# Kernel tuning notes

Measured on AMD Instinct MI355X. Metric: run time of the kernel, lower is better.

Reference implementation:

```python
import jax, jax.numpy as jnp
import numpy as np

NUM_GRAPHS = 4096
EPS = 1e-6

def _ln(x, g, b):
    mu = jnp.mean(x, axis=-1, keepdims=True)
    var = jnp.mean(jnp.square(x - mu), axis=-1, keepdims=True)
    return (x - mu) * jax.lax.rsqrt(var + EPS) * g + b

def setup_inputs() -> dict:
    key = jax.random.key(0)
    ks = jax.random.split(key, 8)
    N, D, H, DRUG = 262144, 128, 8, 128
    feat = jax.random.normal(ks[0], (N, D), dtype=jnp.float32)
    batch = jnp.sort(jax.random.randint(ks[1], (N,), 0, NUM_GRAPHS)).astype(jnp.int64)
    def lin(k, fi, fo):
        lim = 1.0 / np.sqrt(fi)
        return jax.random.uniform(k, (fi, fo), jnp.float32, -lim, lim)
    return {
        'feat': feat, 'batch': batch,
        'W1': lin(ks[2], D, 64), 'b1': jnp.zeros((64,), jnp.float32),
        'g1': jnp.ones((64,), jnp.float32), 'beta1': jnp.zeros((64,), jnp.float32),
        'W2': lin(ks[3], 64, H), 'b2': jnp.zeros((H,), jnp.float32),
        'W3': lin(ks[4], H * D, D), 'b3': jnp.zeros((D,), jnp.float32),
        'g3': jnp.ones((D,), jnp.float32), 'beta3': jnp.zeros((D,), jnp.float32),
        'W4': lin(ks[5], D, DRUG), 'b4': jnp.zeros((DRUG,), jnp.float32),
        'g4': jnp.ones((DRUG,), jnp.float32), 'beta4': jnp.zeros((DRUG,), jnp.float32),
    }

def reference(feat, batch, W1, b1, g1, beta1, W2, b2, W3, b3, g3, beta3, W4, b4, g4, beta4):
    seg = batch.astype(jnp.int32)
    # ATFC: Linear -> LeakyReLU -> LayerNorm -> Linear
    h = jax.nn.leaky_relu(feat @ W1 + b1)
    h = _ln(h, g1, beta1)
    att = jnp.exp(h @ W2 + b2)                      # [N, H]
    # segment softmax normalization
    s = jax.ops.segment_sum(att, seg, num_segments=NUM_GRAPHS)  # [B, H]
    att = att / s[seg]
    # weighted aggregation: outer product + segment sum -> [B, H, D]
    out = jax.ops.segment_sum(att[:, :, None] * feat[:, None, :], seg, num_segments=NUM_GRAPHS)
    out = out.reshape(NUM_GRAPHS, -1)               # [B, H*D]
    # output block (dropout is identity in eval mode)
    o = _ln(jax.nn.leaky_relu(out @ W3 + b3), g3, beta3)
    o = _ln(jax.nn.leaky_relu(o @ W4 + b4), g4, beta4)
    return o
```

## Files before the change

### kernel.cpp

```cpp
#include <hip/hip_runtime.h>
#include <math.h>

#define NG 4096
#define NN 262144
#define D 128
#define M1 64
#define NH 8
#define EPS 1e-6f

typedef __attribute__((ext_vector_type(8))) short short8;
typedef __attribute__((ext_vector_type(8))) unsigned char uchar8;
typedef __attribute__((ext_vector_type(4))) float f32x4;

__device__ inline float leaky(float x) { return x > 0.f ? x : 0.01f * x; }

__device__ inline short f2bf(float f) {
  union { float f; unsigned u; } v; v.f = f;
  unsigned r = (v.u + 0x7fffu + ((v.u >> 16) & 1u)) >> 16;
  return (short)r;
}
__device__ inline float bf2f(short s) {
  union { unsigned u; float f; } v;
  v.u = ((unsigned)(unsigned short)s) << 16;
  return v.f;
}

__global__ __launch_bounds__(256) void k0b_prep(
    const float* __restrict__ W3, const float* __restrict__ W4,
    short* __restrict__ W3T, short* __restrict__ W4T) {
  __shared__ float tile[64][65];
  int b = blockIdx.x, t = threadIdx.x;
  const float* src; short* dst; int kt, nt, tkl;
  if (b < 32) { src = W3; dst = W3T; kt = b >> 1; nt = b & 1; tkl = 1024; }
  else        { src = W4; dst = W4T; kt = (b - 32) >> 1; nt = (b - 32) & 1; tkl = 128; }

#pragma unroll
  for (int i = 0; i < 4; ++i) {
    int id = t + 256 * i;
    int r = id >> 4, c4 = (id & 15) * 4;
    float4 v = *(const float4*)(src + (size_t)(kt * 64 + r) * D + nt * 64 + c4);
    tile[r][c4 + 0] = v.x; tile[r][c4 + 1] = v.y;
    tile[r][c4 + 2] = v.z; tile[r][c4 + 3] = v.w;
  }
  __syncthreads();
  int n = t >> 2, kb = (t & 3) * 16;
  short8 p0, p1;
#pragma unroll
  for (int j = 0; j < 8; ++j) {
    p0[j] = f2bf(tile[kb + j][n]);
    p1[j] = f2bf(tile[kb + 8 + j][n]);
  }
  short* o = dst + (size_t)(nt * 64 + n) * tkl + kt * 64 + kb;
  *(short8*)o = p0;
  *(short8*)(o + 8) = p1;
}

__global__ __launch_bounds__(256) void k1_fused(
    const float* __restrict__ feat, const int* __restrict__ batch,
    const float* __restrict__ W1, const float* __restrict__ b1,
    const float* __restrict__ g1, const float* __restrict__ beta1,
    const float* __restrict__ W2, const float* __restrict__ b2,
    float* __restrict__ out_acc, float* __restrict__ s_sum) {
  __shared__ short W1T[M1][D + 8];
  __shared__ short W2T[16][M1 + 8];
  __shared__ short hb[128][72];
  __shared__ int batchL[128];
  __shared__ unsigned char giL[128];
  short (*attB)[136] = (short(*)[136])&hb[0][0];

  int t = threadIdx.x;
  int nb = blockIdx.x * 128;

#pragma unroll
  for (int i = 0; i < 8; ++i) {
    int idx4 = t + 256 * i;
    int k = idx4 >> 4;
    int j = (idx4 & 15) * 4;
    float4 wv = *(const float4*)(W1 + k * M1 + j);
    W1T[j + 0][k] = f2bf(wv.x);
    W1T[j + 1][k] = f2bf(wv.y);
    W1T[j + 2][k] = f2bf(wv.z);
    W1T[j + 3][k] = f2bf(wv.w);
  }
#pragma unroll
  for (int i = 0; i < 4; ++i) {
    int e = t * 4 + i;
    int hh = e >> 6, j = e & 63;
    W2T[hh][j] = (hh < NH) ? f2bf(W2[j * NH + hh]) : (short)0;
  }
  if (t < 128) batchL[t] = batch[nb + t];
  __syncthreads();

  int w = t >> 6, l = t & 63;
  int lr = l & 15, lq = l >> 4;
  int nbw = nb + w * 32;
  int g_lo = batchL[0], g_hi = batchL[127];

  short8 afr[2][4];
#pragma unroll
  for (int mt = 0; mt < 2; ++mt) {
    const float* rp = feat + (size_t)(nbw + mt * 16 + lr) * D + lq * 8;
#pragma unroll
    for (int c = 0; c < 4; ++c) {
      float4 x0 = *(const float4*)(rp + c * 32);
      float4 x1 = *(const float4*)(rp + c * 32 + 4);
      short8 a;
      a[0] = f2bf(x0.x); a[1] = f2bf(x0.y); a[2] = f2bf(x0.z); a[3] = f2bf(x0.w);
      a[4] = f2bf(x1.x); a[5] = f2bf(x1.y); a[6] = f2bf(x1.z); a[7] = f2bf(x1.w);
      afr[mt][c] = a;
    }
  }

  f32x4 acc[2][4];
#pragma unroll
  for (int mt = 0; mt < 2; ++mt)
#pragma unroll
    for (int nt = 0; nt < 4; ++nt) acc[mt][nt] = (f32x4){0.f, 0.f, 0.f, 0.f};
#pragma unroll
  for (int c = 0; c < 4; ++c) {
#pragma unroll
    for (int nt = 0; nt < 4; ++nt) {
      short8 bfr = *(const short8*)&W1T[nt * 16 + lr][c * 32 + lq * 8];
      acc[0][nt] = __builtin_amdgcn_mfma_f32_16x16x32_bf16(afr[0][c], bfr, acc[0][nt], 0, 0, 0);
      acc[1][nt] = __builtin_amdgcn_mfma_f32_16x16x32_bf16(afr[1][c], bfr, acc[1][nt], 0, 0, 0);
    }
  }

  float b1v[4], g1v[4], btv[4];
#pragma unroll
  for (int nt = 0; nt < 4; ++nt) {
    b1v[nt] = b1[nt * 16 + lr];
    g1v[nt] = g1[nt * 16 + lr];
    btv[nt] = beta1[nt * 16 + lr];
  }
#pragma unroll
  for (int mt = 0; mt < 2; ++mt) {
#pragma unroll
    for (int r = 0; r < 4; ++r) {
      float x[4], s1 = 0.f, s2 = 0.f;
#pragma unroll
      for (int nt = 0; nt < 4; ++nt) {
        float xv = leaky(acc[mt][nt][r] + b1v[nt]);
        x[nt] = xv;
        s1 += xv;
        s2 = fmaf(xv, xv, s2);
      }
#pragma unroll
      for (int off = 1; off < 16; off <<= 1) {
        s1 += __shfl_xor(s1, off);
        s2 += __shfl_xor(s2, off);
      }
      float mu = s1 * (1.f / M1);
      float var = s2 * (1.f / M1) - mu * mu;
      float inv = rsqrtf(var + EPS);
      int node = w * 32 + mt * 16 + lq * 4 + r;
#pragma unroll
      for (int nt = 0; nt < 4; ++nt)
        hb[node][nt * 16 + lr] = f2bf((x[nt] - mu) * inv * g1v[nt] + btv[nt]);
    }
  }
  __syncthreads();

  f32x4 acc2[2];
  acc2[0] = (f32x4){0.f, 0.f, 0.f, 0.f};
  acc2[1] = (f32x4){0.f, 0.f, 0.f, 0.f};
#pragma unroll
  for (int c2 = 0; c2 < 2; ++c2) {
    short8 bfr2 = *(const short8*)&W2T[lr][c2 * 32 + lq * 8];
#pragma unroll
    for (int mt = 0; mt < 2; ++mt) {
      short8 af2 = *(const short8*)&hb[w * 32 + mt * 16 + lr][c2 * 32 + lq * 8];
      acc2[mt] = __builtin_amdgcn_mfma_f32_16x16x32_bf16(af2, bfr2, acc2[mt], 0, 0, 0);
    }
  }
  __syncthreads();

  if (lr < NH) {
    float b2v = b2[lr];
    float attv[2][4];
    int bnode[2][4];
#pragma unroll
    for (int mt = 0; mt < 2; ++mt)
#pragma unroll
      for (int r = 0; r < 4; ++r) {
        int node = w * 32 + mt * 16 + lq * 4 + r;
        float av = bf2f(f2bf(expf(acc2[mt][r] + b2v)));
        attv[mt][r] = av;
        bnode[mt][r] = batchL[node];
        attB[lr][node] = f2bf(av);
      }
    for (int g = g_lo; g <= g_hi; ++g) {
      float ss = 0.f;
#pragma unroll
      for (int mt = 0; mt < 2; ++mt)
#pragma unroll
        for (int r = 0; r < 4; ++r)
          ss += (bnode[mt][r] == g) ? attv[mt][r] : 0.f;
      ss += __shfl_xor(ss, 16);
      ss += __shfl_xor(ss, 32);
      if (lq == 0) atomicAdd(s_sum + g * NH + lr, ss);
    }
  }
  if (t < 128) giL[t] = (unsigned char)(batchL[t] - g_lo);
  __syncthreads();

  short8 bfA[4], bfB[4];
#pragma unroll
  for (int kc = 0; kc < 4; ++kc) {
    int dA = w * 32 + lr, dB = w * 32 + 16 + lr;
    short8 ba, bb;
#pragma unroll
    for (int j = 0; j < 8; ++j) {
      const float* fp = feat + (size_t)(nb + kc * 32 + lq * 8 + j) * D;
      ba[j] = f2bf(fp[dA]);
      bb[j] = f2bf(fp[dB]);
    }
    bfA[kc] = ba;
    bfB[kc] = bb;
  }

  int hA = lr & 7;
  for (int gp = g_lo; gp <= g_hi; gp += 4) {
    int t0 = (gp - g_lo) + (lr >> 3);
    int t1 = t0 + 2;
    f32x4 aggc00 = (f32x4){0.f, 0.f, 0.f, 0.f};
    f32x4 aggc01 = (f32x4){0.f, 0.f, 0.f, 0.f};
    f32x4 aggc10 = (f32x4){0.f, 0.f, 0.f, 0.f};
    f32x4 aggc11 = (f32x4){0.f, 0.f, 0.f, 0.f};
#pragma unroll
    for (int kc = 0; kc < 4; ++kc) {
      short8 av = *(const short8*)&attB[hA][kc * 32 + lq * 8];
      uchar8 gv = *(const uchar8*)&giL[kc * 32 + lq * 8];
      short8 a0, a1;
#pragma unroll
      for (int j = 0; j < 8; ++j) {
        short x = av[j];
        a0[j] = (gv[j] == t0) ? x : (short)0;
        a1[j] = (gv[j] == t1) ? x : (short)0;
      }
      aggc00 = __builtin_amdgcn_mfma_f32_16x16x32_bf16(a0, bfA[kc], aggc00, 0, 0, 0);
      aggc01 = __builtin_amdgcn_mfma_f32_16x16x32_bf16(a0, bfB[kc], aggc01, 0, 0, 0);
      aggc10 = __builtin_amdgcn_mfma_f32_16x16x32_bf16(a1, bfA[kc], aggc10, 0, 0, 0);
      aggc11 = __builtin_amdgcn_mfma_f32_16x16x32_bf16(a1, bfB[kc], aggc11, 0, 0, 0);
    }

    int giC0 = gp + (lq >> 1);
    int giC1 = gp + 2 + (lq >> 1);
    int dA = w * 32 + lr, dB = w * 32 + 16 + lr;
    if (giC0 <= g_hi) {
      float* p0 = out_acc + (size_t)giC0 * (NH * D) + ((lq & 1) * 4) * D;
#pragma unroll
      for (int r = 0; r < 4; ++r) {
        atomicAdd(p0 + r * D + dA, aggc00[r]);
        atomicAdd(p0 + r * D + dB, aggc01[r]);
      }
    }
    if (giC1 <= g_hi) {
      float* p1 = out_acc + (size_t)giC1 * (NH * D) + ((lq & 1) * 4) * D;
#pragma unroll
      for (int r = 0; r < 4; ++r) {
        atomicAdd(p1 + r * D + dA, aggc10[r]);
        atomicAdd(p1 + r * D + dB, aggc11[r]);
      }
    }
  }
}

__global__ __launch_bounds__(128) void k3_mlp(
    const float* __restrict__ X, const float* __restrict__ s_sum,
    const short* __restrict__ W3T,
    const float* __restrict__ b3, const float* __restrict__ g3,
    const float* __restrict__ beta3, const short* __restrict__ W4T,
    const float* __restrict__ b4, const float* __restrict__ g4,
    const float* __restrict__ beta4, float* __restrict__ out) {
  __shared__ short hbuf[16][136];
  __shared__ float red[2][2][16];

  int t = threadIdx.x;
  int nw = t >> 6, l = t & 63;
  int lr = l & 15, lq = l >> 4;
  int gb = blockIdx.x * 16;

  float invs[8];
#pragma unroll
  for (int h = 0; h < 8; ++h) {
    float sv = s_sum[(gb + lr) * NH + h];
    invs[h] = sv > 0.f ? 1.f / sv : 0.f;
  }

  const float* xrow = X + (size_t)(gb + lr) * (NH * D) + lq * 8;
  f32x4 acc[4];
#pragma unroll
  for (int nt = 0; nt < 4; ++nt) acc[nt] = (f32x4){0.f, 0.f, 0.f, 0.f};

#pragma unroll
  for (int kc = 0; kc < 32; ++kc) {
    float4 x0 = *(const float4*)(xrow + kc * 32);
    float4 x1 = *(const float4*)(xrow + kc * 32 + 4);
    float inv = invs[kc >> 2];
    short8 a;
    a[0] = f2bf(x0.x * inv); a[1] = f2bf(x0.y * inv);
    a[2] = f2bf(x0.z * inv); a[3] = f2bf(x0.w * inv);
    a[4] = f2bf(x1.x * inv); a[5] = f2bf(x1.y * inv);
    a[6] = f2bf(x1.z * inv); a[7] = f2bf(x1.w * inv);
#pragma unroll
    for (int nt = 0; nt < 4; ++nt) {
      int ncol = nw * 64 + nt * 16 + lr;
      short8 b = *(const short8*)(W3T + (size_t)ncol * 1024 + kc * 32 + lq * 8);
      acc[nt] = __builtin_amdgcn_mfma_f32_16x16x32_bf16(a, b, acc[nt], 0, 0, 0);
    }
  }

  float xv[4][4], s1[4] = {0.f, 0.f, 0.f, 0.f}, s2[4] = {0.f, 0.f, 0.f, 0.f};
#pragma unroll
  for (int nt = 0; nt < 4; ++nt) {
    float bb = b3[nw * 64 + nt * 16 + lr];
#pragma unroll
    for (int r = 0; r < 4; ++r) {
      float v = leaky(acc[nt][r] + bb);
      xv[nt][r] = v;
      s1[r] += v;
      s2[r] = fmaf(v, v, s2[r]);
    }
  }
#pragma unroll
  for (int off = 1; off < 16; off <<= 1) {
#pragma unroll
    for (int r = 0; r < 4; ++r) {
      s1[r] += __shfl_xor(s1[r], off);
      s2[r] += __shfl_xor(s2[r], off);
    }
  }
  if (lr == 0) {
#pragma unroll
    for (int r = 0; r < 4; ++r) {
      red[nw][0][lq * 4 + r] = s1[r];
      red[nw][1][lq * 4 + r] = s2[r];
    }
  }
  __syncthreads();
#pragma unroll
  for (int nt = 0; nt < 4; ++nt) {
    int col = nw * 64 + nt * 16 + lr;
    float gg = g3[col], bt = beta3[col];
#pragma unroll
    for (int r = 0; r < 4; ++r) {
      int row = lq * 4 + r;
      float S1 = red[0][0][row] + red[1][0][row];
      float S2 = red[0][1][row] + red[1][1][row];
      float mu = S1 * (1.f / D);
      float var = S2 * (1.f / D) - mu * mu;
      float inv = rsqrtf(var + EPS);
      hbuf[row][col] = f2bf((xv[nt][r] - mu) * inv * gg + bt);
    }
  }
  __syncthreads();

  f32x4 acc2[4];
#pragma unroll
  for (int nt = 0; nt < 4; ++nt) acc2[nt] = (f32x4){0.f, 0.f, 0.f, 0.f};
#pragma unroll
  for (int kc = 0; kc < 4; ++kc) {
    short8 a2 = *(const short8*)&hbuf[lr][kc * 32 + lq * 8];
#pragma unroll
    for (int nt = 0; nt < 4; ++nt) {
      int ncol = nw * 64 + nt * 16 + lr;
      short8 b2 = *(const short8*)(W4T + (size_t)ncol * 128 + kc * 32 + lq * 8);
      acc2[nt] = __builtin_amdgcn_mfma_f32_16x16x32_bf16(a2, b2, acc2[nt], 0, 0, 0);
    }
  }

#pragma unroll
  for (int r = 0; r < 4; ++r) { s1[r] = 0.f; s2[r] = 0.f; }
#pragma unroll
  for (int nt = 0; nt < 4; ++nt) {
    float bb = b4[nw * 64 + nt * 16 + lr];
#pragma unroll
    for (int r = 0; r < 4; ++r) {
      float v = leaky(acc2[nt][r] + bb);
      xv[nt][r] = v;
      s1[r] += v;
      s2[r] = fmaf(v, v, s2[r]);
    }
  }
#pragma unroll
  for (int off = 1; off < 16; off <<= 1) {
#pragma unroll
    for (int r = 0; r < 4; ++r) {
      s1[r] += __shfl_xor(s1[r], off);
      s2[r] += __shfl_xor(s2[r], off);
    }
  }
  __syncthreads();
  if (lr == 0) {
#pragma unroll
    for (int r = 0; r < 4; ++r) {
      red[nw][0][lq * 4 + r] = s1[r];
      red[nw][1][lq * 4 + r] = s2[r];
    }
  }
  __syncthreads();
#pragma unroll
  for (int nt = 0; nt < 4; ++nt) {
    int col = nw * 64 + nt * 16 + lr;
    float gg = g4[col], bt = beta4[col];
#pragma unroll
    for (int r = 0; r < 4; ++r) {
      int row = lq * 4 + r;
      float S1 = red[0][0][row] + red[1][0][row];
      float S2 = red[0][1][row] + red[1][1][row];
      float mu = S1 * (1.f / D);
      float var = S2 * (1.f / D) - mu * mu;
      float inv = rsqrtf(var + EPS);
      out[(size_t)(gb + row) * D + col] = (xv[nt][r] - mu) * inv * gg + bt;
    }
  }
}

extern "C" void kernel_launch(void* const* d_in, const int* in_sizes, int n_in,
                              void* d_out, int out_size, void* d_ws, size_t ws_size,
                              hipStream_t stream) {
  (void)in_sizes; (void)n_in; (void)out_size; (void)ws_size;
  const float* feat  = (const float*)d_in[0];
  const int*   batch = (const int*)d_in[1];
  const float* W1    = (const float*)d_in[2];
  const float* b1    = (const float*)d_in[3];
  const float* g1    = (const float*)d_in[4];
  const float* beta1 = (const float*)d_in[5];
  const float* W2    = (const float*)d_in[6];
  const float* b2    = (const float*)d_in[7];
  const float* W3    = (const float*)d_in[8];
  const float* b3    = (const float*)d_in[9];
  const float* g3    = (const float*)d_in[10];
  const float* beta3 = (const float*)d_in[11];
  const float* W4    = (const float*)d_in[12];
  const float* b4    = (const float*)d_in[13];
  const float* g4    = (const float*)d_in[14];
  const float* beta4 = (const float*)d_in[15];
  float* out = (float*)d_out;

  char* ws = (char*)d_ws;
  float* out_acc = (float*)ws;
  float* s_sum   = (float*)(ws + (size_t)NG * NH * D * 4);
  char*  p       = ws + (size_t)NG * NH * D * 4 + (size_t)NG * NH * 4;
  short* W3T     = (short*)p;
  short* W4T     = (short*)(p + 262144);

  hipMemsetAsync(out_acc, 0, (size_t)NG * NH * D * 4 + (size_t)NG * NH * 4,
                 stream);
  k0b_prep<<<36, 256, 0, stream>>>(W3, W4, W3T, W4T);
  k1_fused<<<NN / 128, 256, 0, stream>>>(feat, batch, W1, b1, g1, beta1, W2, b2,
                                         out_acc, s_sum);
  k3_mlp<<<NG / 16, 128, 0, stream>>>(out_acc, s_sum, W3T, b3, g3, beta3, W4T,
                                      b4, g4, beta4, out);
}
```

Baseline: 261.4 us.

## Fuse segment aggregation and output MLP into one graph-partitioned kernel

Each block now owns 8 graphs, with segment start offsets found by binary search in the prep kernel. It walks that range's nodes in 128-node chunks and accumulates the softmax sums and the weighted aggregation in shared memory instead of global atomics. The W3/W4 MLP with its LayerNorms then runs in the same block, which removes the memset, the global out_acc round trip and a separate kernel launch. The cost is a large shared-memory footprint (about 34KB for agg alone), only 512 blocks, and chunk boundaries that do not line up with 128-node tiles, which leads to some redundant loads and padded work.

Result: slower. 268.0 us (+2.5%).

```diff
diff --git a/kernel.cpp b/kernel.cpp
--- a/kernel.cpp
+++ b/kernel.cpp
@@ -6,6 +6,7 @@
 #define D 128
 #define M1 64
 #define NH 8
+#define GPB 8
 #define EPS 1e-6f
 
 typedef __attribute__((ext_vector_type(8))) short short8;
@@ -27,9 +28,22 @@
 
 __global__ __launch_bounds__(256) void k0b_prep(
     const float* __restrict__ W3, const float* __restrict__ W4,
-    short* __restrict__ W3T, short* __restrict__ W4T) {
+    const int* __restrict__ batch,
+    short* __restrict__ W3T, short* __restrict__ W4T,
+    int* __restrict__ starts) {
   __shared__ float tile[64][65];
   int b = blockIdx.x, t = threadIdx.x;
+  if (b >= 36) {
+    int g = (b - 36) * 256 + t;
+    int lo = 0, hi = NN;
+    while (lo < hi) {
+      int mid = (lo + hi) >> 1;
+      if (batch[mid] < g) lo = mid + 1; else hi = mid;
+    }
+    starts[g] = lo;
+    if (g == 0) starts[NG] = NN;
+    return;
+  }
   const float* src; short* dst; int kt, nt, tkl;
   if (b < 32) { src = W3; dst = W3T; kt = b >> 1; nt = b & 1; tkl = 1024; }
   else        { src = W4; dst = W4T; kt = (b - 32) >> 1; nt = (b - 32) & 1; tkl = 128; }
@@ -55,27 +69,38 @@
   *(short8*)(o + 8) = p1;
 }
 
-__global__ __launch_bounds__(256) void k1_fused(
+__global__ __launch_bounds__(256, 2) void k_fused(
     const float* __restrict__ feat, const int* __restrict__ batch,
+    const int* __restrict__ starts,
     const float* __restrict__ W1, const float* __restrict__ b1,
     const float* __restrict__ g1, const float* __restrict__ beta1,
     const float* __restrict__ W2, const float* __restrict__ b2,
-    float* __restrict__ out_acc, float* __restrict__ s_sum) {
+    const short* __restrict__ W3T, const float* __restrict__ b3,
+    const float* __restrict__ g3, const float* __restrict__ beta3,
+    const short* __restrict__ W4T, const float* __restrict__ b4,
+    const float* __restrict__ g4, const float* __restrict__ beta4,
+    float* __restrict__ out) {
   __shared__ short W1T[M1][D + 8];
   __shared__ short W2T[16][M1 + 8];
   __shared__ short hb[128][72];
-  __shared__ int batchL[128];
-  __shared__ unsigned char giL[128];
+  __shared__ float agg[GPB][NH][D + 4];
+  __shared__ float sL[GPB][NH];
+  __shared__ unsigned char giL2[2][128];
+  __shared__ float red[4][2][16];
+  __shared__ short hbuf2[16][136];
+
   short (*attB)[136] = (short(*)[136])&hb[0][0];
+  short (*aL)[1040] = (short(*)[1040])&hb[0][0];
 
   int t = threadIdx.x;
-  int nb = blockIdx.x * 128;
+  int G0 = blockIdx.x * GPB;
+  int w = t >> 6, l = t & 63;
+  int lr = l & 15, lq = l >> 4;
 
 #pragma unroll
   for (int i = 0; i < 8; ++i) {
     int idx4 = t + 256 * i;
-    int k = idx4 >> 4;
-    int j = (idx4 & 15) * 4;
+    int k = idx4 >> 4, j = (idx4 & 15) * 4;
     float4 wv = *(const float4*)(W1 + k * M1 + j);
     W1T[j + 0][k] = f2bf(wv.x);
     W1T[j + 1][k] = f2bf(wv.y);
@@ -88,43 +113,8 @@
     int hh = e >> 6, j = e & 63;
     W2T[hh][j] = (hh < NH) ? f2bf(W2[j * NH + hh]) : (short)0;
   }
-  if (t < 128) batchL[t] = batch[nb + t];
-  __syncthreads();
-
-  int w = t >> 6, l = t & 63;
-  int lr = l & 15, lq = l >> 4;
-  int nbw = nb + w * 32;
-  int g_lo = batchL[0], g_hi = batchL[127];
-
-  short8 afr[2][4];
-#pragma unroll
-  for (int mt = 0; mt < 2; ++mt) {
-    const float* rp = feat + (size_t)(nbw + mt * 16 + lr) * D + lq * 8;
-#pragma unroll
-    for (int c = 0; c < 4; ++c) {
-      float4 x0 = *(const float4*)(rp + c * 32);
-      float4 x1 = *(const float4*)(rp + c * 32 + 4);
-      short8 a;
-      a[0] = f2bf(x0.x); a[1] = f2bf(x0.y); a[2] = f2bf(x0.z); a[3] = f2bf(x0.w);
-      a[4] = f2bf(x1.x); a[5] = f2bf(x1.y); a[6] = f2bf(x1.z); a[7] = f2bf(x1.w);
-      afr[mt][c] = a;
-    }
-  }
-
-  f32x4 acc[2][4];
-#pragma unroll
-  for (int mt = 0; mt < 2; ++mt)
-#pragma unroll
-    for (int nt = 0; nt < 4; ++nt) acc[mt][nt] = (f32x4){0.f, 0.f, 0.f, 0.f};
-#pragma unroll
-  for (int c = 0; c < 4; ++c) {
-#pragma unroll
-    for (int nt = 0; nt < 4; ++nt) {
-      short8 bfr = *(const short8*)&W1T[nt * 16 + lr][c * 32 + lq * 8];
-      acc[0][nt] = __builtin_amdgcn_mfma_f32_16x16x32_bf16(afr[0][c], bfr, acc[0][nt], 0, 0, 0);
-      acc[1][nt] = __builtin_amdgcn_mfma_f32_16x16x32_bf16(afr[1][c], bfr, acc[1][nt], 0, 0, 0);
-    }
-  }
+  for (int i = t; i < GPB * NH * (D + 4); i += 256) (&agg[0][0][0])[i] = 0.f;
+  if (t < GPB * NH) (&sL[0][0])[t] = 0.f;
 
   float b1v[4], g1v[4], btv[4];
 #pragma unroll
@@ -133,286 +123,311 @@
     g1v[nt] = g1[nt * 16 + lr];
     btv[nt] = beta1[nt * 16 + lr];
   }
-#pragma unroll
-  for (int mt = 0; mt < 2; ++mt) {
-#pragma unroll
-    for (int r = 0; r < 4; ++r) {
-      float x[4], s1 = 0.f, s2 = 0.f;
+  float b2v = b2[lr & 7];
+
+  int s0 = starts[G0], s1 = starts[G0 + GPB];
+  int nchunks = (s1 - s0 + 127) >> 7;
+
+  for (int c = 0; c < nchunks; ++c) {
+    int base = s0 + (c << 7);
+    int nvalid = min(128, s1 - base);
+    unsigned char* gi = giL2[c & 1];
+    if (t < 128)
+      gi[t] = (t < nvalid) ? (unsigned char)(batch[base + t] - G0)
+                           : (unsigned char)255;
+
+    short8 afr[2][4];
+#pragma unroll
+    for (int mt = 0; mt < 2; ++mt) {
+      int node = base + w * 32 + mt * 16 + lr;
+      node = node < NN ? node : NN - 1;
+      const float* rp = feat + (size_t)node * D + lq * 8;
+#pragma unroll
+      for (int cc = 0; cc < 4; ++cc) {
+        float4 x0 = *(const float4*)(rp + cc * 32);
+        float4 x1 = *(const float4*)(rp + cc * 32 + 4);
+        short8 a;
+        a[0] = f2bf(x0.x); a[1] = f2bf(x0.y); a[2] = f2bf(x0.z); a[3] = f2bf(x0.w);
+        a[4] = f2bf(x1.x); a[5] = f2bf(x1.y); a[6] = f2bf(x1.z); a[7] = f2bf(x1.w);
+        afr[mt][cc] = a;
+      }
+    }
+    __syncthreads();
+
+    f32x4 acc[2][4];
+#pragma unroll
+    for (int mt = 0; mt < 2; ++mt)
+#pragma unroll
+      for (int nt = 0; nt < 4; ++nt) acc[mt][nt] = (f32x4){0.f, 0.f, 0.f, 0.f};
+#pragma unroll
+    for (int cc = 0; cc < 4; ++cc) {
 #pragma unroll
       for (int nt = 0; nt < 4; ++nt) {
-        float xv = leaky(acc[mt][nt][r] + b1v[nt]);
-        x[nt] = xv;
-        s1 += xv;
-        s2 = fmaf(xv, xv, s2);
-      }
-#pragma unroll
-      for (int off = 1; off < 16; off <<= 1) {
-        s1 += __shfl_xor(s1, off);
-        s2 += __shfl_xor(s2, off);
-      }
-      float mu = s1 * (1.f / M1);
-      float var = s2 * (1.f / M1) - mu * mu;
-      float inv = rsqrtf(var + EPS);
-      int node = w * 32 + mt * 16 + lq * 4 + r;
-#pragma unroll
-      for (int nt = 0; nt < 4; ++nt)
-        hb[node][nt * 16 + lr] = f2bf((x[nt] - mu) * inv * g1v[nt] + btv[nt]);
-    }
-  }
-  __syncthreads();
-
-  f32x4 acc2[2];
-  acc2[0] = (f32x4){0.f, 0.f, 0.f, 0.f};
-  acc2[1] = (f32x4){0.f, 0.f, 0.f, 0.f};
-#pragma unroll
-  for (int c2 = 0; c2 < 2; ++c2) {
-    short8 bfr2 = *(const short8*)&W2T[lr][c2 * 32 + lq * 8];
+        short8 bfr = *(const short8*)&W1T[nt * 16 + lr][cc * 32 + lq * 8];
+        acc[0][nt] = __builtin_amdgcn_mfma_f32_16x16x32_bf16(afr[0][cc], bfr, acc[0][nt], 0, 0, 0);
+        acc[1][nt] = __builtin_amdgcn_mfma_f32_16x16x32_bf16(afr[1][cc], bfr, acc[1][nt], 0, 0, 0);
+      }
+    }
+
 #pragma unroll
     for (int mt = 0; mt < 2; ++mt) {
-      short8 af2 = *(const short8*)&hb[w * 32 + mt * 16 + lr][c2 * 32 + lq * 8];
-      acc2[mt] = __builtin_amdgcn_mfma_f32_16x16x32_bf16(af2, bfr2, acc2[mt], 0, 0, 0);
-    }
-  }
-  __syncthreads();
-
-  if (lr < NH) {
-    float b2v = b2[lr];
-    float attv[2][4];
-    int bnode[2][4];
-#pragma unroll
-    for (int mt = 0; mt < 2; ++mt)
 #pragma unroll
       for (int r = 0; r < 4; ++r) {
+        float x[4], sa = 0.f, sb = 0.f;
+#pragma unroll
+        for (int nt = 0; nt < 4; ++nt) {
+          float xvv = leaky(acc[mt][nt][r] + b1v[nt]);
+          x[nt] = xvv; sa += xvv; sb = fmaf(xvv, xvv, sb);
+        }
+#pragma unroll
+        for (int off = 1; off < 16; off <<= 1) {
+          sa += __shfl_xor(sa, off);
+          sb += __shfl_xor(sb, off);
+        }
+        float mu = sa * (1.f / M1);
+        float var = sb * (1.f / M1) - mu * mu;
+        float inv = rsqrtf(var + EPS);
         int node = w * 32 + mt * 16 + lq * 4 + r;
-        float av = bf2f(f2bf(expf(acc2[mt][r] + b2v)));
-        attv[mt][r] = av;
-        bnode[mt][r] = batchL[node];
-        attB[lr][node] = f2bf(av);
-      }
-    for (int g = g_lo; g <= g_hi; ++g) {
-      float ss = 0.f;
+#pragma unroll
+        for (int nt = 0; nt < 4; ++nt)
+          hb[node][nt * 16 + lr] = f2bf((x[nt] - mu) * inv * g1v[nt] + btv[nt]);
+      }
+    }
+    __syncthreads();
+
+    f32x4 acc2[2];
+    acc2[0] = (f32x4){0.f, 0.f, 0.f, 0.f};
+    acc2[1] = (f32x4){0.f, 0.f, 0.f, 0.f};
+#pragma unroll
+    for (int c2 = 0; c2 < 2; ++c2) {
+      short8 bfr2 = *(const short8*)&W2T[lr][c2 * 32 + lq * 8];
+#pragma unroll
+      for (int mt = 0; mt < 2; ++mt) {
+        short8 af2 = *(const short8*)&hb[w * 32 + mt * 16 + lr][c2 * 32 + lq * 8];
+        acc2[mt] = __builtin_amdgcn_mfma_f32_16x16x32_bf16(af2, bfr2, acc2[mt], 0, 0, 0);
+      }
+    }
+    __syncthreads();
+
+    int gl_lo = gi[0];
+    int gl_hi = gi[nvalid - 1];
+
+    if (lr < NH) {
+      float attv[2][4];
+      int gnode[2][4];
 #pragma unroll
       for (int mt = 0; mt < 2; ++mt)
 #pragma unroll
-        for (int r = 0; r < 4; ++r)
-          ss += (bnode[mt][r] == g) ? attv[mt][r] : 0.f;
-      ss += __shfl_xor(ss, 16);
-      ss += __shfl_xor(ss, 32);
-      if (lq == 0) atomicAdd(s_sum + g * NH + lr, ss);
-    }
-  }
-  if (t < 128) giL[t] = (unsigned char)(batchL[t] - g_lo);
-  __syncthreads();
-
-  short8 bfA[4], bfB[4];
-#pragma unroll
-  for (int kc = 0; kc < 4; ++kc) {
-    int dA = w * 32 + lr, dB = w * 32 + 16 + lr;
-    short8 ba, bb;
-#pragma unroll
-    for (int j = 0; j < 8; ++j) {
-      const float* fp = feat + (size_t)(nb + kc * 32 + lq * 8 + j) * D;
-      ba[j] = f2bf(fp[dA]);
-      bb[j] = f2bf(fp[dB]);
-    }
-    bfA[kc] = ba;
-    bfB[kc] = bb;
-  }
-
-  int hA = lr & 7;
-  for (int gp = g_lo; gp <= g_hi; gp += 4) {
-    int t0 = (gp - g_lo) + (lr >> 3);
-    int t1 = t0 + 2;
-    f32x4 aggc00 = (f32x4){0.f, 0.f, 0.f, 0.f};
-    f32x4 aggc01 = (f32x4){0.f, 0.f, 0.f, 0.f};
-    f32x4 aggc10 = (f32x4){0.f, 0.f, 0.f, 0.f};
-    f32x4 aggc11 = (f32x4){0.f, 0.f, 0.f, 0.f};
+        for (int r = 0; r < 4; ++r) {
+          int node = w * 32 + mt * 16 + lq * 4 + r;
+          float av = bf2f(f2bf(expf(acc2[mt][r] + b2v)));
+          attv[mt][r] = av;
+          gnode[mt][r] = gi[node];
+          attB[lr][node] = f2bf(av);
+        }
+      for (int g = gl_lo; g <= gl_hi; ++g) {
+        float ss = 0.f;
+#pragma unroll
+        for (int mt = 0; mt < 2; ++mt)
+#pragma unroll
+          for (int r = 0; r < 4; ++r)
+            ss += (gnode[mt][r] == g) ? attv[mt][r] : 0.f;
+        ss += __shfl_xor(ss, 16);
+        ss += __shfl_xor(ss, 32);
+        if (lq == 0) atomicAdd(&sL[g][lr], ss);
+      }
+    }
+    __syncthreads();
+
+    int dA = w * 32 + lr, dB = dA + 16;
+    short8 bfA[4], bfB[4];
 #pragma unroll
     for (int kc = 0; kc < 4; ++kc) {
-      short8 av = *(const short8*)&attB[hA][kc * 32 + lq * 8];
-      uchar8 gv = *(const uchar8*)&giL[kc * 32 + lq * 8];
-      short8 a0, a1;
+      short8 ba, bb;
 #pragma unroll
       for (int j = 0; j < 8; ++j) {
-        short x = av[j];
-        a0[j] = (gv[j] == t0) ? x : (short)0;
-        a1[j] = (gv[j] == t1) ? x : (short)0;
-      }
-      aggc00 = __builtin_amdgcn_mfma_f32_16x16x32_bf16(a0, bfA[kc], aggc00, 0, 0, 0);
-      aggc01 = __builtin_amdgcn_mfma_f32_16x16x32_bf16(a0, bfB[kc], aggc01, 0, 0, 0);
-      aggc10 = __builtin_amdgcn_mfma_f32_16x16x32_bf16(a1, bfA[kc], aggc10, 0, 0, 0);
-      aggc11 = __builtin_amdgcn_mfma_f32_16x16x32_bf16(a1, bfB[kc], aggc11, 0, 0, 0);
-    }
-
-    int giC0 = gp + (lq >> 1);
-    int giC1 = gp + 2 + (lq >> 1);
-    int dA = w * 32 + lr, dB = w * 32 + 16 + lr;
-    if (giC0 <= g_hi) {
-      float* p0 = out_acc + (size_t)giC0 * (NH * D) + ((lq & 1) * 4) * D;
-#pragma unroll
-      for (int r = 0; r < 4; ++r) {
-        atomicAdd(p0 + r * D + dA, aggc00[r]);
-        atomicAdd(p0 + r * D + dB, aggc01[r]);
-      }
-    }
-    if (giC1 <= g_hi) {
-      float* p1 = out_acc + (size_t)giC1 * (NH * D) + ((lq & 1) * 4) * D;
-#pragma unroll
-      for (int r = 0; r < 4; ++r) {
-        atomicAdd(p1 + r * D + dA, aggc10[r]);
-        atomicAdd(p1 + r * D + dB, aggc11[r]);
-      }
-    }
-  }
-}
-
-__global__ __launch_bounds__(128) void k3_mlp(
-    const float* __restrict__ X, const float* __restrict__ s_sum,
-    const short* __restrict__ W3T,
-    const float* __restrict__ b3, const float* __restrict__ g3,
-    const float* __restrict__ beta3, const short* __restrict__ W4T,
-    const float* __restrict__ b4, const float* __restrict__ g4,
-    const float* __restrict__ beta4, float* __restrict__ out) {
-  __shared__ short hbuf[16][136];
-  __shared__ float red[2][2][16];
-
-  int t = threadIdx.x;
-  int nw = t >> 6, l = t & 63;
-  int lr = l & 15, lq = l >> 4;
-  int gb = blockIdx.x * 16;
-
-  float invs[8];
-#pragma unroll
-  for (int h = 0; h < 8; ++h) {
-    float sv = s_sum[(gb + lr) * NH + h];
-    invs[h] = sv > 0.f ? 1.f / sv : 0.f;
-  }
-
-  const float* xrow = X + (size_t)(gb + lr) * (NH * D) + lq * 8;
-  f32x4 acc[4];
-#pragma unroll
-  for (int nt = 0; nt < 4; ++nt) acc[nt] = (f32x4){0.f, 0.f, 0.f, 0.f};
-
+        int node = base + kc * 32 + lq * 8 + j;
+        node = node < NN ? node : NN - 1;
+        const float* fp = feat + (size_t)node * D;
+        ba[j] = f2bf(fp[dA]);
+        bb[j] = f2bf(fp[dB]);
+      }
+      bfA[kc] = ba;
+      bfB[kc] = bb;
+    }
+
+    int hA = lr & 7;
+    for (int gp = gl_lo; gp <= gl_hi; gp += 4) {
+      int t0 = gp + (lr >> 3);
+      int t1 = t0 + 2;
+      f32x4 c00 = (f32x4){0.f, 0.f, 0.f, 0.f};
+      f32x4 c01 = (f32x4){0.f, 0.f, 0.f, 0.f};
+      f32x4 c10 = (f32x4){0.f, 0.f, 0.f, 0.f};
+      f32x4 c11 = (f32x4){0.f, 0.f, 0.f, 0.f};
+#pragma unroll
+      for (int kc = 0; kc < 4; ++kc) {
+        short8 av = *(const short8*)&attB[hA][kc * 32 + lq * 8];
+        uchar8 gv = *(const uchar8*)&gi[kc * 32 + lq * 8];
+        short8 a0, a1;
+#pragma unroll
+        for (int j = 0; j < 8; ++j) {
+          short x = av[j];
+          a0[j] = (gv[j] == t0) ? x : (short)0;
+          a1[j] = (gv[j] == t1) ? x : (short)0;
+        }
+        c00 = __builtin_amdgcn_mfma_f32_16x16x32_bf16(a0, bfA[kc], c00, 0, 0, 0);
+        c01 = __builtin_amdgcn_mfma_f32_16x16x32_bf16(a0, bfB[kc], c01, 0, 0, 0);
+        c10 = __builtin_amdgcn_mfma_f32_16x16x32_bf16(a1, bfA[kc], c10, 0, 0, 0);
+        c11 = __builtin_amdgcn_mfma_f32_16x16x32_bf16(a1, bfB[kc], c11, 0, 0, 0);
+      }
+      int giC0 = gp + (lq >> 1);
+      int giC1 = giC0 + 2;
+      int hC = (lq & 1) * 4;
+      if (giC0 < GPB) {
+#pragma unroll
+        for (int r = 0; r < 4; ++r) {
+          agg[giC0][hC + r][dA] += c00[r];
+          agg[giC0][hC + r][dB] += c01[r];
+        }
+      }
+      if (giC1 < GPB) {
+#pragma unroll
+        for (int r = 0; r < 4; ++r) {
+          agg[giC1][hC + r][dA] += c10[r];
+          agg[giC1][hC + r][dB] += c11[r];
+        }
+      }
+    }
+  }
+  __syncthreads();
+
+  if (t < GPB * NH) {
+    float sv = (&sL[0][0])[t];
+    (&sL[0][0])[t] = sv > 0.f ? 1.f / sv : 0.f;
+  }
+  __syncthreads();
+
+  for (int i = t; i < GPB * NH * D; i += 256) {
+    int gi2 = i >> 10;
+    int k = i & 1023;
+    int h = k >> 7, d = k & 127;
+    aL[gi2][k] = f2bf(agg[gi2][h][d] * sL[gi2][h]);
+  }
+  __syncthreads();
+
+  int ar = lr & 7;
+  f32x4 acc3[2];
+  acc3[0] = (f32x4){0.f, 0.f, 0.f, 0.f};
+  acc3[1] = (f32x4){0.f, 0.f, 0.f, 0.f};
 #pragma unroll
   for (int kc = 0; kc < 32; ++kc) {
-    float4 x0 = *(const float4*)(xrow + kc * 32);
-    float4 x1 = *(const float4*)(xrow + kc * 32 + 4);
-    float inv = invs[kc >> 2];
-    short8 a;
-    a[0] = f2bf(x0.x * inv); a[1] = f2bf(x0.y * inv);
-    a[2] = f2bf(x0.z * inv); a[3] = f2bf(x0.w * inv);
-    a[4] = f2bf(x1.x * inv); a[5] = f2bf(x1.y * inv);
-    a[6] = f2bf(x1.z * inv); a[7] = f2bf(x1.w * inv);
-#pragma unroll
-    for (int nt = 0; nt < 4; ++nt) {
-      int ncol = nw * 64 + nt * 16 + lr;
+    short8 a = *(const short8*)&aL[ar][kc * 32 + lq * 8];
+#pragma unroll
+    for (int nt = 0; nt < 2; ++nt) {
+      int ncol = w * 32 + nt * 16 + lr;
       short8 b = *(const short8*)(W3T + (size_t)ncol * 1024 + kc * 32 + lq * 8);
-      acc[nt] = __builtin_amdgcn_mfma_f32_16x16x32_bf16(a, b, acc[nt], 0, 0, 0);
-    }
-  }
-
-  float xv[4][4], s1[4] = {0.f, 0.f, 0.f, 0.f}, s2[4] = {0.f, 0.f, 0.f, 0.f};
-#pragma unroll
-  for (int nt = 0; nt < 4; ++nt) {
-    float bb = b3[nw * 64 + nt * 16 + lr];
-#pragma unroll
-    for (int r = 0; r < 4; ++r) {
-      float v = leaky(acc[nt][r] + bb);
+      acc3[nt] = __builtin_amdgcn_mfma_f32_16x16x32_bf16(a, b, acc3[nt], 0, 0, 0);
+    }
+  }
+
+  float xv[2][4], sa[4] = {0.f, 0.f, 0.f, 0.f}, sb[4] = {0.f, 0.f, 0.f, 0.f};
+#pragma unroll
+  for (int nt = 0; nt < 2; ++nt) {
+    float bb = b3[w * 32 + nt * 16 + lr];
+#pragma unroll
+    for (int r = 0; r < 4; ++r) {
+      float v = leaky(acc3[nt][r] + bb);
       xv[nt][r] = v;
-      s1[r] += v;
-      s2[r] = fmaf(v, v, s2[r]);
-    }
-  }
-#pragma unroll
-  for (int off = 1; off < 16; off <<= 1) {
-#pragma unroll
-    for (int r = 0; r < 4; ++r) {
-      s1[r] += __shfl_xor(s1[r], off);
-      s2[r] += __shfl_xor(s2[r], off);
-    }
-  }
-  if (lr == 0) {
-#pragma unroll
-    for (int r = 0; r < 4; ++r) {
-      red[nw][0][lq * 4 + r] = s1[r];
-      red[nw][1][lq * 4 + r] = s2[r];
-    }
-  }
-  __syncthreads();
-#pragma unroll
-  for (int nt = 0; nt < 4; ++nt) {
-    int col = nw * 64 + nt * 16 + lr;
+      sa[r] += v;
+      sb[r] = fmaf(v, v, sb[r]);
+    }
+  }
+#pragma unroll
+  for (int off = 1; off < 16; off <<= 1)
+#pragma unroll
+    for (int r = 0; r < 4; ++r) {
+      sa[r] += __shfl_xor(sa[r], off);
+      sb[r] += __shfl_xor(sb[r], off);
+    }
+  if (lr == 0)
+#pragma unroll
+    for (int r = 0; r < 4; ++r) {
+      red[w][0][lq * 4 + r] = sa[r];
+      red[w][1][lq * 4 + r] = sb[r];
+    }
+  __syncthreads();
+#pragma unroll
+  for (int nt = 0; nt < 2; ++nt) {
+    int col = w * 32 + nt * 16 + lr;
     float gg = g3[col], bt = beta3[col];
 #pragma unroll
     for (int r = 0; r < 4; ++r) {
       int row = lq * 4 + r;
-      float S1 = red[0][0][row] + red[1][0][row];
-      float S2 = red[0][1][row] + red[1][1][row];
+      float S1 = red[0][0][row] + red[1][0][row] + red[2][0][row] + red[3][0][row];
+      float S2 = red[0][1][row] + red[1][1][row] + red[2][1][row] + red[3][1][row];
       float mu = S1 * (1.f / D);
       float var = S2 * (1.f / D) - mu * mu;
       float inv = rsqrtf(var + EPS);
-      hbuf[row][col] = f2bf((xv[nt][r] - mu) * inv * gg + bt);
-    }
-  }
-  __syncthreads();
-
-  f32x4 acc2[4];
-#pragma unroll
-  for (int nt = 0; nt < 4; ++nt) acc2[nt] = (f32x4){0.f, 0.f, 0.f, 0.f};
+      hbuf2[row][col] = f2bf((xv[nt][r] - mu) * inv * gg + bt);
+    }
+  }
+  __syncthreads();
+
+  f32x4 acc4[2];
+  acc4[0] = (f32x4){0.f, 0.f, 0.f, 0.f};
+  acc4[1] = (f32x4){0.f, 0.f, 0.f, 0.f};
 #pragma unroll
   for (int kc = 0; kc < 4; ++kc) {
-    short8 a2 = *(const short8*)&hbuf[lr][kc * 32 + lq * 8];
-#pragma unroll
-    for (int nt = 0; nt < 4; ++nt) {
-      int ncol = nw * 64 + nt * 16 + lr;
-      short8 b2 = *(const short8*)(W4T + (size_t)ncol * 128 + kc * 32 + lq * 8);
-      acc2[nt] = __builtin_amdgcn_mfma_f32_16x16x32_bf16(a2, b2, acc2[nt], 0, 0, 0);
-    }
-  }
-
-#pragma unroll
-  for (int r = 0; r < 4; ++r) { s1[r] = 0.f; s2[r] = 0.f; }
-#pragma unroll
-  for (int nt = 0; nt < 4; ++nt) {
-    float bb = b4[nw * 64 + nt * 16 + lr];
-#pragma unroll
-    for (int r = 0; r < 4; ++r) {
-      float v = leaky(acc2[nt][r] + bb);
+    short8 a2 = *(const short8*)&hbuf2[lr][kc * 32 + lq * 8];
+#pragma unroll
+    for (int nt = 0; nt < 2; ++nt) {
+      int ncol = w * 32 + nt * 16 + lr;
+      short8 b4f = *(const short8*)(W4T + (size_t)ncol * 128 + kc * 32 + lq * 8);
+      acc4[nt] = __builtin_amdgcn_mfma_f32_16x16x32_bf16(a2, b4f, acc4[nt], 0, 0, 0);
+    }
+  }
+#pragma unroll
+  for (int r = 0; r < 4; ++r) { sa[r] = 0.f; sb[r] = 0.f; }
+#pragma unroll
+  for (int nt = 0; nt < 2; ++nt) {
+    float bb = b4[w * 32 + nt * 16 + lr];
+#pragma unroll
+    for (int r = 0; r < 4; ++r) {
+      float v = leaky(acc4[nt][r] + bb);
       xv[nt][r] = v;
-      s1[r] += v;
-      s2[r] = fmaf(v, v, s2[r]);
-    }
-  }
-#pragma unroll
-  for (int off = 1; off < 16; off <<= 1) {
-#pragma unroll
-    for (int r = 0; r < 4; ++r) {
-      s1[r] += __shfl_xor(s1[r], off);
-      s2[r] += __shfl_xor(s2[r], off);
-    }
-  }
-  __syncthreads();
-  if (lr == 0) {
-#pragma unroll
-    for (int r = 0; r < 4; ++r) {
-      red[nw][0][lq * 4 + r] = s1[r];
-      red[nw][1][lq * 4 + r] = s2[r];
-    }
-  }
-  __syncthreads();
-#pragma unroll
-  for (int nt = 0; nt < 4; ++nt) {
-    int col = nw * 64 + nt * 16 + lr;
+      sa[r] += v;
+      sb[r] = fmaf(v, v, sb[r]);
+    }
+  }
+#pragma unroll
+  for (int off = 1; off < 16; off <<= 1)
+#pragma unroll
+    for (int r = 0; r < 4; ++r) {
+      sa[r] += __shfl_xor(sa[r], off);
+      sb[r] += __shfl_xor(sb[r], off);
+    }
+  if (lr == 0)
+#pragma unroll
+    for (int r = 0; r < 4; ++r) {
+      red[w][0][lq * 4 + r] = sa[r];
+      red[w][1][lq * 4 + r] = sb[r];
+    }
+  __syncthreads();
+#pragma unroll
+  for (int nt = 0; nt < 2; ++nt) {
+    int col = w * 32 + nt * 16 + lr;
     float gg = g4[col], bt = beta4[col];
 #pragma unroll
     for (int r = 0; r < 4; ++r) {
       int row = lq * 4 + r;
-      float S1 = red[0][0][row] + red[1][0][row];
-      float S2 = red[0][1][row] + red[1][1][row];
-      float mu = S1 * (1.f / D);
-      float var = S2 * (1.f / D) - mu * mu;
-      float inv = rsqrtf(var + EPS);
-      out[(size_t)(gb + row) * D + col] = (xv[nt][r] - mu) * inv * gg + bt;
+      if (row < GPB) {
+        float S1 = red[0][0][row] + red[1][0][row] + red[2][0][row] + red[3][0][row];
+        float S2 = red[0][1][row] + red[1][1][row] + red[2][1][row] + red[3][1][row];
+        float mu = S1 * (1.f / D);
+        float var = S2 * (1.f / D) - mu * mu;
+        float inv = rsqrtf(var + EPS);
+        out[(size_t)(G0 + row) * D + col] = (xv[nt][r] - mu) * inv * gg + bt;
+      }
     }
   }
 }
@@ -440,17 +455,12 @@
   float* out = (float*)d_out;
 
   char* ws = (char*)d_ws;
-  float* out_acc = (float*)ws;
-  float* s_sum   = (float*)(ws + (size_t)NG * NH * D * 4);
-  char*  p       = ws + (size_t)NG * NH * D * 4 + (size_t)NG * NH * 4;
-  short* W3T     = (short*)p;
-  short* W4T     = (short*)(p + 262144);
-
-  hipMemsetAsync(out_acc, 0, (size_t)NG * NH * D * 4 + (size_t)NG * NH * 4,
-                 stream);
-  k0b_prep<<<36, 256, 0, stream>>>(W3, W4, W3T, W4T);
-  k1_fused<<<NN / 128, 256, 0, stream>>>(feat, batch, W1, b1, g1, beta1, W2, b2,
-                                         out_acc, s_sum);
-  k3_mlp<<<NG / 16, 128, 0, stream>>>(out_acc, s_sum, W3T, b3, g3, beta3, W4T,
-                                      b4, g4, beta4, out);
+  short* W3T   = (short*)ws;
+  short* W4T   = (short*)(ws + 262144);
+  int*  starts = (int*)(ws + 262144 + 32768);
+
+  k0b_prep<<<52, 256, 0, stream>>>(W3, W4, batch, W3T, W4T, starts);
+  k_fused<<<NG / GPB, 256, 0, stream>>>(feat, batch, starts, W1, b1, g1, beta1,
+                                        W2, b2, W3T, b3, g3, beta3, W4T, b4, g4,
+                                        beta4, out);
 }
```
